# Kernel tuning notes

Hardware: AMD Instinct MI355X
Metric: run time of the kernel (lower is better)

The kernel has to match this reference:

```python
import jax, jax.numpy as jnp
import numpy as np

N = 10000      # nodes (docstring: dense mode intended for <=10k nodes)
D_IN = 64      # in_dim
D_OUT = 64     # out_dim


def setup_inputs() -> dict:
    key = jax.random.key(0)
    kH, kA1, kA2, kA3, kW1, kW2, kW3 = jax.random.split(key, 7)
    H = jax.random.normal(kH, (N, D_IN), dtype=jnp.float32)
    # Dense normalized adjacency per edge type (values in [0,1), as in A_norm)
    A_r1 = jax.random.uniform(kA1, (N, N), dtype=jnp.float32)
    A_r2 = jax.random.uniform(kA2, (N, N), dtype=jnp.float32)
    A_r3 = jax.random.uniform(kA3, (N, N), dtype=jnp.float32)
    # Xavier-uniform init for type-specific linear weights [out_dim, in_dim]
    limit = float(np.sqrt(6.0 / (D_IN + D_OUT)))
    W1 = jax.random.uniform(kW1, (D_OUT, D_IN), dtype=jnp.float32, minval=-limit, maxval=limit)
    W2 = jax.random.uniform(kW2, (D_OUT, D_IN), dtype=jnp.float32, minval=-limit, maxval=limit)
    W3 = jax.random.uniform(kW3, (D_OUT, D_IN), dtype=jnp.float32, minval=-limit, maxval=limit)
    bias = jnp.zeros((D_OUT,), dtype=jnp.float32)
    return {"H": H, "A_r1": A_r1, "A_r2": A_r2, "A_r3": A_r3,
            "W1": W1, "W2": W2, "W3": W3, "bias": bias}


def reference(H, A_r1, A_r2, A_r3, W1, W2, W3, bias):
    # h_v = sum_r W_r @ (sum_u A_r[v,u] * h_u) + b  (no activation in forward)
    out = bias  # broadcasts to [N, D_OUT]
    for A_r, W_r in ((A_r1, W1), (A_r2, W2), (A_r3, W3)):
        msg = A_r @ H                      # [N, D_IN] neighbor aggregation
        out = out + msg @ W_r.T            # [N, D_OUT] type-specific projection
    return out
```

## Files before the change

### kernel.cpp

```cpp
#include <hip/hip_runtime.h>

static constexpr int NN = 10000;
static constexpr int DD = 64;
static constexpr int KP = 10240;
static constexpr int BK = 128;
static constexpr int SPLITS = 4;
static constexpr int KC = KP / SPLITS;
static constexpr int ITERS = KC / BK;
static constexpr int BM = 64;

typedef __attribute__((ext_vector_type(4))) float f32x4;
typedef __attribute__((ext_vector_type(8))) short s16x8;

__device__ __forceinline__ unsigned short f2bf(float f) {
  unsigned u = __float_as_uint(f);
  return (unsigned short)((u + 0x7fffu + ((u >> 16) & 1u)) >> 16);
}

__device__ __forceinline__ void g2l16(const void* g, void* l) {
  __builtin_amdgcn_global_load_lds((const __attribute__((address_space(1))) unsigned int*)g,
                                   (__attribute__((address_space(3))) unsigned int*)l, 16, 0, 0);
}

__global__ void prep_kernel(const float* __restrict__ H,
                            const float* __restrict__ W1,
                            const float* __restrict__ W2,
                            const float* __restrict__ W3,
                            unsigned short* __restrict__ mt) {
  const int r = blockIdx.y;
  const float* W = (r == 0) ? W1 : (r == 1) ? W2 : W3;
  const int wave = threadIdx.x >> 6;
  const int lane = threadIdx.x & 63;
  f32x4 wr[16];
#pragma unroll
  for (int i = 0; i < 16; ++i) wr[i] = *(const f32x4*)&W[lane * 64 + i * 4];
  unsigned short* orow = mt + ((size_t)r * 64 + lane) * KP;
  const int kbase = blockIdx.x * 128 + wave * 32;
  for (int i = 0; i < 32; ++i) {
    const int k = kbase + i;
    if (k < NN) {
      float s = 0.f;
#pragma unroll
      for (int j = 0; j < 16; ++j) {
        f32x4 h = *(const f32x4*)&H[(size_t)k * 64 + j * 4];
        s += h[0] * wr[j][0] + h[1] * wr[j][1] + h[2] * wr[j][2] + h[3] * wr[j][3];
      }
      orow[k] = f2bf(s);
    } else {
      orow[k] = 0;
    }
  }
}

__global__ void init_out_kernel(const float* __restrict__ bias, float* __restrict__ out) {
  const int i = blockIdx.x * 256 + threadIdx.x;
  if (i < NN * DD) out[i] = bias[i & 63];
}

__global__ __launch_bounds__(256, 4) void gcn_main(const float* __restrict__ A1,
                                                   const float* __restrict__ A2,
                                                   const float* __restrict__ A3,
                                                   const unsigned short* __restrict__ mt,
                                                   float* __restrict__ out) {
  __shared__ __align__(1024) unsigned short mlds[2][64][128];

  const int r = blockIdx.z;
  const int s = blockIdx.y;
  const float* A = (r == 0) ? A1 : (r == 1) ? A2 : A3;
  const unsigned short* mtr = mt + (size_t)r * 64 * KP;

  const int wave = threadIdx.x >> 6;
  const int lane = threadIdx.x & 63;
  const int l15 = lane & 15;
  const int lhi = lane >> 4;
  const int seg = lane & 15;
  const int r16 = lane >> 4;
  const int v0 = blockIdx.x * BM;
  const int k0 = s * KC;

  int vA = v0 + wave * 16 + l15;
  if (vA > NN - 1) vA = NN - 1;
  const float* arow = A + (size_t)vA * NN;

  f32x4 acc[4] = {{0.f,0.f,0.f,0.f},{0.f,0.f,0.f,0.f},{0.f,0.f,0.f,0.f},{0.f,0.f,0.f,0.f}};
  f32x4 aF[4][2], aN[4][2];

  auto stageM = [&](int t, int buf) {
    const int kb = k0 + t * BK;
#pragma unroll
    for (int j = 0; j < 4; ++j) {
      const int row16 = 4 * j + r16;
      const int rowabs = wave * 16 + row16;
      const unsigned short* src = mtr + (size_t)rowabs * KP + kb + ((seg ^ row16) << 3);
      g2l16(src, &mlds[buf][wave * 16 + 4 * j][0]);
    }
  };
  auto loadA = [&](f32x4 (&a)[4][2], int kb) {
    const bool guard = (kb + BK > NN);
#pragma unroll
    for (int kk = 0; kk < 4; ++kk) {
      const int kf = kb + kk * 32 + lhi * 8;
      if (!guard) {
        a[kk][0] = *(const f32x4*)(arow + kf);
        a[kk][1] = *(const f32x4*)(arow + kf + 4);
      } else {
        f32x4 z = {0.f, 0.f, 0.f, 0.f};
        if (kf < NN) {
          a[kk][0] = *(const f32x4*)(arow + kf);
          a[kk][1] = *(const f32x4*)(arow + kf + 4);
        } else {
          a[kk][0] = z; a[kk][1] = z;
        }
      }
    }
  };
  auto cvtA = [&](const f32x4& x, const f32x4& y) -> s16x8 {
    s16x8 v;
    v[0] = (short)f2bf(x[0]); v[1] = (short)f2bf(x[1]);
    v[2] = (short)f2bf(x[2]); v[3] = (short)f2bf(x[3]);
    v[4] = (short)f2bf(y[0]); v[5] = (short)f2bf(y[1]);
    v[6] = (short)f2bf(y[2]); v[7] = (short)f2bf(y[3]);
    return v;
  };

  stageM(0, 0);
  loadA(aF, k0);
  __syncthreads();

  for (int t = 0; t < ITERS; ++t) {
    const int buf = t & 1;
    const bool pref = (t + 1 < ITERS);
    if (pref) {
      loadA(aN, k0 + (t + 1) * BK);
      stageM(t + 1, buf ^ 1);
    }
#pragma unroll
    for (int kk = 0; kk < 4; ++kk) {
      s16x8 a = cvtA(aF[kk][0], aF[kk][1]);
#pragma unroll
      for (int dt = 0; dt < 4; ++dt) {
        const int rrow = dt * 16 + l15;
        const int g = kk * 4 + lhi;
        s16x8 b = *(const s16x8*)&mlds[buf][rrow][((g ^ l15) & 15) * 8];
        acc[dt] = __builtin_amdgcn_mfma_f32_16x16x32_bf16(a, b, acc[dt], 0, 0, 0);
      }
    }
    __syncthreads();
    if (pref) {
#pragma unroll
      for (int kk = 0; kk < 4; ++kk) { aF[kk][0] = aN[kk][0]; aF[kk][1] = aN[kk][1]; }
    }
  }

#pragma unroll
  for (int dt = 0; dt < 4; ++dt) {
    const int d = dt * 16 + l15;
#pragma unroll
    for (int i = 0; i < 4; ++i) {
      const int v = v0 + wave * 16 + lhi * 4 + i;
      if (v < NN) atomicAdd(&out[(size_t)v * DD + d], acc[dt][i]);
    }
  }
}

extern "C" void kernel_launch(void* const* d_in, const int* in_sizes, int n_in,
                              void* d_out, int out_size, void* d_ws, size_t ws_size,
                              hipStream_t stream) {
  const float* H    = (const float*)d_in[0];
  const float* A1   = (const float*)d_in[1];
  const float* A2   = (const float*)d_in[2];
  const float* A3   = (const float*)d_in[3];
  const float* W1   = (const float*)d_in[4];
  const float* W2   = (const float*)d_in[5];
  const float* W3   = (const float*)d_in[6];
  const float* bias = (const float*)d_in[7];
  float* out = (float*)d_out;
  unsigned short* mt = (unsigned short*)d_ws;

  prep_kernel<<<dim3(KP / 128, 3), 256, 0, stream>>>(H, W1, W2, W3, mt);
  init_out_kernel<<<dim3((NN * DD + 255) / 256), 256, 0, stream>>>(bias, out);
  gcn_main<<<dim3((NN + BM - 1) / BM, SPLITS, 3), 256, 0, stream>>>(A1, A2, A3, mt, out);
}
```

Measured before the change: 323.7 us.

## Hand-issue A loads via inline asm with explicit vmcnt waits and ping-pong registers

Replaces the compiler-generated prefetch of the fp32 A tiles with inline-asm global_load_dwordx4 instructions. Each iteration issues the next tile's A loads and LDS staging, then waits with s_waitcnt vmcnt(12) and raw s_barrier instead of full __syncthreads. The loop is unrolled by two with ping-pong register buffers, which removes the register copy between iterations. Boundary tails are handled by clamping addresses and zeroing afterwards. The goal is to keep more memory traffic in flight and cut waits on the bandwidth-bound A stream. The risk is that the compiler does not know the asm outputs arrive late, so it could move or copy those registers before the wait.

Result: faster. 310.1 us (-4.2%).

```diff
diff --git a/kernel.cpp b/kernel.cpp
--- a/kernel.cpp
+++ b/kernel.cpp
@@ -83,7 +83,7 @@
   const float* arow = A + (size_t)vA * NN;
 
   f32x4 acc[4] = {{0.f,0.f,0.f,0.f},{0.f,0.f,0.f,0.f},{0.f,0.f,0.f,0.f},{0.f,0.f,0.f,0.f}};
-  f32x4 aF[4][2], aN[4][2];
+  f32x4 R0[4][2], R1[4][2];
 
   auto stageM = [&](int t, int buf) {
     const int kb = k0 + t * BK;
@@ -95,25 +95,47 @@
       g2l16(src, &mlds[buf][wave * 16 + 4 * j][0]);
     }
   };
-  auto loadA = [&](f32x4 (&a)[4][2], int kb) {
-    const bool guard = (kb + BK > NN);
-#pragma unroll
-    for (int kk = 0; kk < 4; ++kk) {
-      const int kf = kb + kk * 32 + lhi * 8;
-      if (!guard) {
-        a[kk][0] = *(const f32x4*)(arow + kf);
-        a[kk][1] = *(const f32x4*)(arow + kf + 4);
-      } else {
-        f32x4 z = {0.f, 0.f, 0.f, 0.f};
-        if (kf < NN) {
-          a[kk][0] = *(const f32x4*)(arow + kf);
-          a[kk][1] = *(const f32x4*)(arow + kf + 4);
-        } else {
-          a[kk][0] = z; a[kk][1] = z;
-        }
-      }
-    }
-  };
+
+  auto issueA = [&](f32x4 (&a)[4][2], int kb) {
+    if (kb + BK <= NN) {
+      const float* p = arow + kb + lhi * 8;
+      asm volatile(
+        "global_load_dwordx4 %0, %8, off\n\t"
+        "global_load_dwordx4 %1, %8, off offset:16\n\t"
+        "global_load_dwordx4 %2, %8, off offset:128\n\t"
+        "global_load_dwordx4 %3, %8, off offset:144\n\t"
+        "global_load_dwordx4 %4, %8, off offset:256\n\t"
+        "global_load_dwordx4 %5, %8, off offset:272\n\t"
+        "global_load_dwordx4 %6, %8, off offset:384\n\t"
+        "global_load_dwordx4 %7, %8, off offset:400"
+        : "=&v"(a[0][0]), "=&v"(a[0][1]), "=&v"(a[1][0]), "=&v"(a[1][1]),
+          "=&v"(a[2][0]), "=&v"(a[2][1]), "=&v"(a[3][0]), "=&v"(a[3][1])
+        : "v"(p));
+    } else {
+      const int kf0 = kb + lhi * 8;
+      const float* q0 = arow + ((kf0       < NN) ? kf0       : 0);
+      const float* q1 = arow + ((kf0 + 4   < NN) ? kf0 + 4   : 0);
+      const float* q2 = arow + ((kf0 + 32  < NN) ? kf0 + 32  : 0);
+      const float* q3 = arow + ((kf0 + 36  < NN) ? kf0 + 36  : 0);
+      const float* q4 = arow + ((kf0 + 64  < NN) ? kf0 + 64  : 0);
+      const float* q5 = arow + ((kf0 + 68  < NN) ? kf0 + 68  : 0);
+      const float* q6 = arow + ((kf0 + 96  < NN) ? kf0 + 96  : 0);
+      const float* q7 = arow + ((kf0 + 100 < NN) ? kf0 + 100 : 0);
+      asm volatile(
+        "global_load_dwordx4 %0, %8, off\n\t"
+        "global_load_dwordx4 %1, %9, off\n\t"
+        "global_load_dwordx4 %2, %10, off\n\t"
+        "global_load_dwordx4 %3, %11, off\n\t"
+        "global_load_dwordx4 %4, %12, off\n\t"
+        "global_load_dwordx4 %5, %13, off\n\t"
+        "global_load_dwordx4 %6, %14, off\n\t"
+        "global_load_dwordx4 %7, %15, off"
+        : "=&v"(a[0][0]), "=&v"(a[0][1]), "=&v"(a[1][0]), "=&v"(a[1][1]),
+          "=&v"(a[2][0]), "=&v"(a[2][1]), "=&v"(a[3][0]), "=&v"(a[3][1])
+        : "v"(q0), "v"(q1), "v"(q2), "v"(q3), "v"(q4), "v"(q5), "v"(q6), "v"(q7));
+    }
+  };
+
   auto cvtA = [&](const f32x4& x, const f32x4& y) -> s16x8 {
     s16x8 v;
     v[0] = (short)f2bf(x[0]); v[1] = (short)f2bf(x[1]);
@@ -123,34 +145,48 @@
     return v;
   };
 
-  stageM(0, 0);
-  loadA(aF, k0);
-  __syncthreads();
-
-  for (int t = 0; t < ITERS; ++t) {
+  auto body = [&](int t, f32x4 (&cur)[4][2], f32x4 (&nxt)[4][2]) {
+    const int tn = (t + 1 < ITERS) ? t + 1 : ITERS - 1;
+    issueA(nxt, k0 + tn * BK);
+    stageM(tn, (t + 1) & 1);
+    __builtin_amdgcn_sched_barrier(0);
+    asm volatile("s_waitcnt vmcnt(12)");
+    __builtin_amdgcn_sched_barrier(0);
+    __builtin_amdgcn_s_barrier();
+    const int kb = k0 + t * BK;
     const int buf = t & 1;
-    const bool pref = (t + 1 < ITERS);
-    if (pref) {
-      loadA(aN, k0 + (t + 1) * BK);
-      stageM(t + 1, buf ^ 1);
+    if (kb + BK > NN) {
+      const f32x4 z = {0.f, 0.f, 0.f, 0.f};
+#pragma unroll
+      for (int kk = 0; kk < 4; ++kk) {
+        const int kf = kb + kk * 32 + lhi * 8;
+        cur[kk][0] = (kf     >= NN) ? z : cur[kk][0];
+        cur[kk][1] = (kf + 4 >= NN) ? z : cur[kk][1];
+      }
     }
 #pragma unroll
     for (int kk = 0; kk < 4; ++kk) {
-      s16x8 a = cvtA(aF[kk][0], aF[kk][1]);
+      s16x8 a = cvtA(cur[kk][0], cur[kk][1]);
 #pragma unroll
       for (int dt = 0; dt < 4; ++dt) {
-        const int rrow = dt * 16 + l15;
         const int g = kk * 4 + lhi;
-        s16x8 b = *(const s16x8*)&mlds[buf][rrow][((g ^ l15) & 15) * 8];
+        s16x8 b = *(const s16x8*)&mlds[buf][dt * 16 + l15][((g ^ l15) & 15) * 8];
         acc[dt] = __builtin_amdgcn_mfma_f32_16x16x32_bf16(a, b, acc[dt], 0, 0, 0);
       }
     }
-    __syncthreads();
-    if (pref) {
-#pragma unroll
-      for (int kk = 0; kk < 4; ++kk) { aF[kk][0] = aN[kk][0]; aF[kk][1] = aN[kk][1]; }
-    }
+    __builtin_amdgcn_sched_barrier(0);
+    __builtin_amdgcn_s_barrier();
+  };
+
+  issueA(R0, k0);
+  stageM(0, 0);
+
+  for (int t = 0; t < ITERS; t += 2) {
+    body(t, R0, R1);
+    body(t + 1, R1, R0);
   }
+
+  asm volatile("s_waitcnt vmcnt(0)");
 
 #pragma unroll
   for (int dt = 0; dt < 4; ++dt) {
```

## Stage A through LDS with coalesced row-wise loads and inline-asm pipelining

Applied to the files above, without the earlier changes.

A tiles are now loaded row-contiguously by half-waves (32 lanes x 16 bytes per row), which coalesces better than the earlier per-lane 32-byte strided pattern. The tile is converted to bf16, written into a swizzled LDS buffer and read back in MFMA fragment layout. Loads are issued with inline asm, and explicit vmcnt waits plus sched barriers order the global loads against the compute. The cost is extra LDS traffic and a doubled LDS footprint, with launch bounds lowered to 2 blocks per CU. The last iteration redundantly reloads the same tile.

Result: faster. 293.3 us (-9.4%).

```diff
diff --git a/kernel.cpp b/kernel.cpp
--- a/kernel.cpp
+++ b/kernel.cpp
@@ -11,6 +11,7 @@
 
 typedef __attribute__((ext_vector_type(4))) float f32x4;
 typedef __attribute__((ext_vector_type(8))) short s16x8;
+typedef __attribute__((ext_vector_type(4))) unsigned short u16x4;
 
 __device__ __forceinline__ unsigned short f2bf(float f) {
   unsigned u = __float_as_uint(f);
@@ -57,12 +58,13 @@
   if (i < NN * DD) out[i] = bias[i & 63];
 }
 
-__global__ __launch_bounds__(256, 4) void gcn_main(const float* __restrict__ A1,
+__global__ __launch_bounds__(256, 2) void gcn_main(const float* __restrict__ A1,
                                                    const float* __restrict__ A2,
                                                    const float* __restrict__ A3,
                                                    const unsigned short* __restrict__ mt,
                                                    float* __restrict__ out) {
-  __shared__ __align__(1024) unsigned short mlds[2][64][128];
+  __shared__ __align__(1024) unsigned short mldsM[2][64][128];
+  __shared__ __align__(1024) unsigned short mldsA[2][64][128];
 
   const int r = blockIdx.z;
   const int s = blockIdx.y;
@@ -73,83 +75,122 @@
   const int lane = threadIdx.x & 63;
   const int l15 = lane & 15;
   const int lhi = lane >> 4;
-  const int seg = lane & 15;
-  const int r16 = lane >> 4;
+  const int l31 = lane & 31;
+  const int lh5 = lane >> 5;
   const int v0 = blockIdx.x * BM;
   const int k0 = s * KC;
 
-  int vA = v0 + wave * 16 + l15;
-  if (vA > NN - 1) vA = NN - 1;
-  const float* arow = A + (size_t)vA * NN;
+  const float* rowPtr[8];
+  int wOff[8];
+#pragma unroll
+  for (int j = 0; j < 8; ++j) {
+    const int rloc = wave * 16 + 2 * j + lh5;
+    int vr = v0 + rloc; if (vr > NN - 1) vr = NN - 1;
+    rowPtr[j] = A + (size_t)vr * NN;
+    wOff[j] = rloc * 256 + (((l31 >> 1) ^ (rloc & 15)) * 16) + (lane & 1) * 8;
+  }
+  int rOffA[4], rOffM[4][4];
+#pragma unroll
+  for (int kk = 0; kk < 4; ++kk) {
+    rOffA[kk] = (wave * 16 + l15) * 256 + (((kk * 4 + lhi) ^ l15) * 16);
+#pragma unroll
+    for (int dt = 0; dt < 4; ++dt)
+      rOffM[kk][dt] = (dt * 16 + l15) * 256 + (((kk * 4 + lhi) ^ l15) * 16);
+  }
 
   f32x4 acc[4] = {{0.f,0.f,0.f,0.f},{0.f,0.f,0.f,0.f},{0.f,0.f,0.f,0.f},{0.f,0.f,0.f,0.f}};
-  f32x4 aF[4][2], aN[4][2];
+  f32x4 ar[8];
 
   auto stageM = [&](int t, int buf) {
     const int kb = k0 + t * BK;
 #pragma unroll
     for (int j = 0; j < 4; ++j) {
-      const int row16 = 4 * j + r16;
+      const int row16 = 4 * j + (lane >> 4);
       const int rowabs = wave * 16 + row16;
-      const unsigned short* src = mtr + (size_t)rowabs * KP + kb + ((seg ^ row16) << 3);
-      g2l16(src, &mlds[buf][wave * 16 + 4 * j][0]);
+      const unsigned short* src = mtr + (size_t)rowabs * KP + kb + (((lane & 15) ^ row16) << 3);
+      g2l16(src, &mldsM[buf][wave * 16 + 4 * j][0]);
     }
   };
-  auto loadA = [&](f32x4 (&a)[4][2], int kb) {
-    const bool guard = (kb + BK > NN);
-#pragma unroll
-    for (int kk = 0; kk < 4; ++kk) {
-      const int kf = kb + kk * 32 + lhi * 8;
-      if (!guard) {
-        a[kk][0] = *(const f32x4*)(arow + kf);
-        a[kk][1] = *(const f32x4*)(arow + kf + 4);
-      } else {
-        f32x4 z = {0.f, 0.f, 0.f, 0.f};
-        if (kf < NN) {
-          a[kk][0] = *(const f32x4*)(arow + kf);
-          a[kk][1] = *(const f32x4*)(arow + kf + 4);
-        } else {
-          a[kk][0] = z; a[kk][1] = z;
+
+  auto issueA = [&](int kb) {
+    int koff = kb + l31 * 4;
+    if (koff > NN - 4) koff = NN - 4;
+    const float* p0 = rowPtr[0] + koff; const float* p1 = rowPtr[1] + koff;
+    const float* p2 = rowPtr[2] + koff; const float* p3 = rowPtr[3] + koff;
+    const float* p4 = rowPtr[4] + koff; const float* p5 = rowPtr[5] + koff;
+    const float* p6 = rowPtr[6] + koff; const float* p7 = rowPtr[7] + koff;
+    asm volatile(
+      "global_load_dwordx4 %0, %8, off\n\t"
+      "global_load_dwordx4 %1, %9, off\n\t"
+      "global_load_dwordx4 %2, %10, off\n\t"
+      "global_load_dwordx4 %3, %11, off\n\t"
+      "global_load_dwordx4 %4, %12, off\n\t"
+      "global_load_dwordx4 %5, %13, off\n\t"
+      "global_load_dwordx4 %6, %14, off\n\t"
+      "global_load_dwordx4 %7, %15, off"
+      : "=&v"(ar[0]), "=&v"(ar[1]), "=&v"(ar[2]), "=&v"(ar[3]),
+        "=&v"(ar[4]), "=&v"(ar[5]), "=&v"(ar[6]), "=&v"(ar[7])
+      : "v"(p0), "v"(p1), "v"(p2), "v"(p3), "v"(p4), "v"(p5), "v"(p6), "v"(p7));
+  };
+
+  auto cvtWrite = [&](int buf, int kb) {
+    if (kb + BK > NN) {
+      if (kb + l31 * 4 > NN - 4) {
+#pragma unroll
+        for (int j = 0; j < 8; ++j) ar[j] = (f32x4){0.f, 0.f, 0.f, 0.f};
+      }
+    }
+    char* base = (char*)&mldsA[buf][0][0];
+#pragma unroll
+    for (int j = 0; j < 8; ++j) {
+      u16x4 c;
+      c[0] = f2bf(ar[j][0]); c[1] = f2bf(ar[j][1]);
+      c[2] = f2bf(ar[j][2]); c[3] = f2bf(ar[j][3]);
+      *(u16x4*)(base + wOff[j]) = c;
+    }
+  };
+
+  issueA(k0);
+  __builtin_amdgcn_sched_barrier(0);
+  stageM(0, 0);
+  __builtin_amdgcn_sched_barrier(0);
+  asm volatile("s_waitcnt vmcnt(4)");
+  __builtin_amdgcn_sched_barrier(0);
+  cvtWrite(0, k0);
+  __builtin_amdgcn_sched_barrier(0);
+  asm volatile("s_waitcnt vmcnt(0)");
+  __builtin_amdgcn_sched_barrier(0);
+  __builtin_amdgcn_s_barrier();
+
+  for (int t = 0; t < ITERS; ++t) {
+    const int buf = t & 1;
+    const int tn = (t + 1 < ITERS) ? t + 1 : t;
+    const int kbn = k0 + tn * BK;
+    issueA(kbn);
+    __builtin_amdgcn_sched_barrier(0);
+    stageM(tn, buf ^ 1);
+    __builtin_amdgcn_sched_barrier(0);
+    {
+      const char* aBase = (const char*)&mldsA[buf][0][0];
+      const char* mBase = (const char*)&mldsM[buf][0][0];
+#pragma unroll
+      for (int kk = 0; kk < 4; ++kk) {
+        s16x8 a = *(const s16x8*)(aBase + rOffA[kk]);
+#pragma unroll
+        for (int dt = 0; dt < 4; ++dt) {
+          s16x8 b = *(const s16x8*)(mBase + rOffM[kk][dt]);
+          acc[dt] = __builtin_amdgcn_mfma_f32_16x16x32_bf16(a, b, acc[dt], 0, 0, 0);
         }
       }
     }
-  };
-  auto cvtA = [&](const f32x4& x, const f32x4& y) -> s16x8 {
-    s16x8 v;
-    v[0] = (short)f2bf(x[0]); v[1] = (short)f2bf(x[1]);
-    v[2] = (short)f2bf(x[2]); v[3] = (short)f2bf(x[3]);
-    v[4] = (short)f2bf(y[0]); v[5] = (short)f2bf(y[1]);
-    v[6] = (short)f2bf(y[2]); v[7] = (short)f2bf(y[3]);
-    return v;
-  };
-
-  stageM(0, 0);
-  loadA(aF, k0);
-  __syncthreads();
-
-  for (int t = 0; t < ITERS; ++t) {
-    const int buf = t & 1;
-    const bool pref = (t + 1 < ITERS);
-    if (pref) {
-      loadA(aN, k0 + (t + 1) * BK);
-      stageM(t + 1, buf ^ 1);
-    }
-#pragma unroll
-    for (int kk = 0; kk < 4; ++kk) {
-      s16x8 a = cvtA(aF[kk][0], aF[kk][1]);
-#pragma unroll
-      for (int dt = 0; dt < 4; ++dt) {
-        const int rrow = dt * 16 + l15;
-        const int g = kk * 4 + lhi;
-        s16x8 b = *(const s16x8*)&mlds[buf][rrow][((g ^ l15) & 15) * 8];
-        acc[dt] = __builtin_amdgcn_mfma_f32_16x16x32_bf16(a, b, acc[dt], 0, 0, 0);
-      }
-    }
-    __syncthreads();
-    if (pref) {
-#pragma unroll
-      for (int kk = 0; kk < 4; ++kk) { aF[kk][0] = aN[kk][0]; aF[kk][1] = aN[kk][1]; }
-    }
+    __builtin_amdgcn_sched_barrier(0);
+    asm volatile("s_waitcnt vmcnt(4)");
+    __builtin_amdgcn_sched_barrier(0);
+    cvtWrite(buf ^ 1, kbn);
+    __builtin_amdgcn_sched_barrier(0);
+    asm volatile("s_waitcnt vmcnt(0)");
+    __builtin_amdgcn_sched_barrier(0);
+    __builtin_amdgcn_s_barrier();
   }
 
 #pragma unroll
```
